# Optimization experiments

Hardware: AMD Instinct MI355X
Metric: run time of the kernel (lower is better)

## Reference

```python
import jax, jax.numpy as jnp
import numpy as np

NUM_V, NUM_R, ARITY = 100000, 1000, 3
D, I, H = 128, 64, 128
B, N = 4096, 64


def setup_inputs() -> dict:
    key = jax.random.key(0)
    ks = jax.random.split(key, 11)
    return {
        "r": jax.random.randint(ks[0], (B, N), 0, NUM_R),
        "e": jax.random.randint(ks[1], (ARITY, B, N), 0, NUM_V),
        "V": jax.random.normal(ks[2], (NUM_V, D + I), dtype=jnp.float32),
        "R": jax.random.normal(ks[3], (NUM_R, D), dtype=jnp.float32),
        "P": jax.random.normal(ks[4], (ARITY, D), dtype=jnp.float32),
        "WV": jax.random.normal(ks[5], (D + I, H), dtype=jnp.float32) * (1.0 / np.sqrt(D + I)),
        "bV": jax.random.normal(ks[6], (H,), dtype=jnp.float32) * 0.01,
        "WR": jax.random.normal(ks[7], (D, H), dtype=jnp.float32) * (1.0 / np.sqrt(D)),
        "bR": jax.random.normal(ks[8], (H,), dtype=jnp.float32) * 0.01,
        "WP": jax.random.normal(ks[9], (D, H), dtype=jnp.float32) * (1.0 / np.sqrt(D)),
        "bP": jax.random.normal(ks[10], (H,), dtype=jnp.float32) * 0.01,
    }


def reference(r, e, V, R, P, WV, bV, WR, bR, WP, bP):
    # x = Rl(R[r]) : gather relation embeddings then project -> [B, N, H]
    x = jnp.einsum("bnd,dh->bnh", R[r], WR) + bR
    # Pl(P[i]) for all arity positions at once -> [A, H]
    pe = P @ WP + bP
    # Vl(V[e[i]]) for all positions: gather then project -> [A, B, N, H]
    ve = jnp.einsum("abnd,dh->abnh", V[e], WV) + bV
    # loop body x = x * Pl(P[i]) * Vl(V[e[i]]) == product over arity axis
    x = x * jnp.prod(pe[:, None, None, :] * ve, axis=0)
    # dropout is identity (p=0 / eval); reduce over neighbor axis
    return jnp.sum(x, axis=1)  # [B, H]
```

## Files before the change

### kernel.cpp

```cpp
#include <hip/hip_runtime.h>

#define NUM_V 100000
#define NUM_R 1000
#define ARITY 3
#define DD 128
#define DI 192
#define HH 128
#define BB 4096
#define NN 64

typedef __attribute__((ext_vector_type(4))) float f32x4;
typedef __attribute__((ext_vector_type(8))) _Float16 half8;
typedef __attribute__((ext_vector_type(2))) _Float16 half2v;

__global__ __launch_bounds__(832, 6) void gemm_fused(
    const float* __restrict__ A, const float* __restrict__ WV, const float* __restrict__ bV,
    const float* __restrict__ R, const float* __restrict__ WR, const float* __restrict__ bR,
    const float* __restrict__ P, const float* __restrict__ WP, const float* __restrict__ bP,
    _Float16* __restrict__ VWh, _Float16* __restrict__ RWh, float* __restrict__ peProd,
    int M) {
    __shared__ unsigned short bsm[24576];

    const int tid = threadIdx.x;
    const int l = tid & 63;
    const int wv = tid >> 6;
    const int bid = blockIdx.x;

    const int tile = wv * 512 + bid;
    const int rowbase = tile * 16;
    const bool active = rowbase < M;

    float bcol[8];
#pragma unroll
    for (int ct = 0; ct < 8; ++ct) bcol[ct] = bV[ct * 16 + (l & 15)];

    const float* aptr;
    {
        int rr = rowbase + (l & 15);
        if (rr >= M) rr = M - 1;
        aptr = A + (size_t)rr * DI + (l >> 4) * 8;
    }

    f32x4 acc[8];
#pragma unroll
    for (int ct = 0; ct < 8; ++ct) acc[ct] = (f32x4){0.f, 0.f, 0.f, 0.f};

    float4 va[3][2];
#define LOAD_A(buf, ks)                                      \
    do {                                                     \
        va[buf][0] = *(const float4*)(aptr + (ks) * 32);     \
        va[buf][1] = *(const float4*)(aptr + (ks) * 32 + 4); \
    } while (0)

    if (active) {
        LOAD_A(0, 0);
        LOAD_A(1, 1);
    }

    if (tid < 768) {
#pragma unroll
        for (int i = 0; i < 4; ++i) {
            const int g = i * 768 + tid;
            const int ks = g >> 9;
            const int ct = (g >> 6) & 7;
            const int ln = g & 63;
            const int col = ct * 16 + (ln & 15);
            const int kbase = ks * 32 + ((ln >> 4) << 3);
            half8 hv;
#pragma unroll
            for (int j = 0; j < 8; ++j)
                hv[j] = (_Float16)WV[(size_t)(kbase + j) * HH + col];
            *(half8*)&bsm[(size_t)g * 8] = hv;
        }
    }

    __syncthreads();

    if (active) {
#pragma unroll
        for (int ks = 0; ks < 6; ++ks) {
            const int cur = ks % 3;
            if (ks < 4) LOAD_A((ks + 2) % 3, ks + 2);

            half8 ah;
            {
                half8 t;
                t[0] = (_Float16)va[cur][0].x;
                t[1] = (_Float16)va[cur][0].y;
                t[2] = (_Float16)va[cur][0].z;
                t[3] = (_Float16)va[cur][0].w;
                t[4] = (_Float16)va[cur][1].x;
                t[5] = (_Float16)va[cur][1].y;
                t[6] = (_Float16)va[cur][1].z;
                t[7] = (_Float16)va[cur][1].w;
                ah = t;
            }

#pragma unroll
            for (int ct = 0; ct < 8; ++ct) {
                const int fb = (ks * 8 + ct) * 512;
                half8 bh = *(const half8*)&bsm[fb + l * 8];
                acc[ct] = __builtin_amdgcn_mfma_f32_16x16x32_f16(ah, bh, acc[ct], 0, 0, 0);
            }
        }

        const int rb = rowbase + (l >> 4) * 4;
#pragma unroll
        for (int j = 0; j < 4; ++j) {
            const int row = rb + j;
            if (row < M) {
#pragma unroll
                for (int ct = 0; ct < 8; ++ct)
                    VWh[(size_t)row * HH + ct * 16 + (l & 15)] = (_Float16)(acc[ct][j] + bcol[ct]);
            }
        }
    }
#undef LOAD_A

    if (bid < 500) {
        if (tid < 256) {
            const int row = bid * 2 + (tid >> 7);
            const int col = tid & 127;
            float a2 = bR[col];
            const float* Rr = R + (size_t)row * DD;
            for (int d = 0; d < DD; ++d) a2 += Rr[d] * WR[(size_t)d * HH + col];
            RWh[(size_t)row * HH + col] = (_Float16)a2;
        }
    } else if (bid == 511) {
        if (tid < HH) {
            const int h = tid;
            float prod = 1.0f;
            for (int a = 0; a < ARITY; ++a) {
                float a2 = bP[h];
                for (int d = 0; d < DD; ++d) a2 += P[a * DD + d] * WP[d * HH + h];
                prod *= a2;
            }
            peProd[h] = prod;
        }
    }
}

__global__ __launch_bounds__(256) void gather_kernel(const int* __restrict__ r,
                                                     const int* __restrict__ e,
                                                     const _Float16* __restrict__ VWh,
                                                     const _Float16* __restrict__ RWh,
                                                     const float* __restrict__ peProd,
                                                     float* __restrict__ out) {
    __shared__ int rIdx[NN];
    __shared__ int eIdx[ARITY][NN];
    __shared__ float4 partial[3][16][2];

    const int b = blockIdx.x;
    const int tid = threadIdx.x;

    if (tid < NN) {
        rIdx[tid] = r[b * NN + tid];
    } else {
        int t = tid - NN;
        eIdx[t >> 6][t & 63] = e[(size_t)(t >> 6) * BB * NN + b * NN + (t & 63)];
    }
    __syncthreads();

    const int lane = tid & 63;
    const int wv = tid >> 6;
    const int q = lane >> 4;
    const int ho = lane & 15;

    float acc8[8];
#pragma unroll
    for (int k = 0; k < 8; ++k) acc8[k] = 0.f;

#pragma unroll
    for (int it = 0; it < 4; ++it) {
        int n = it * 16 + wv * 4 + q;
        half8 rw = *(const half8*)(RWh + (size_t)rIdx[n] * HH + ho * 8);
        half8 v0 = *(const half8*)(VWh + (size_t)eIdx[0][n] * HH + ho * 8);
        half8 v1 = *(const half8*)(VWh + (size_t)eIdx[1][n] * HH + ho * 8);
        half8 v2 = *(const half8*)(VWh + (size_t)eIdx[2][n] * HH + ho * 8);
        half8 p = rw * v0;
        p = p * v1;
        p = p * v2;
#pragma unroll
        for (int k = 0; k < 8; ++k) acc8[k] += (float)p[k];
    }

#pragma unroll
    for (int k = 0; k < 8; ++k) {
        acc8[k] += __shfl_xor(acc8[k], 16);
        acc8[k] += __shfl_xor(acc8[k], 32);
    }

    if (wv > 0 && lane < 16) {
        partial[wv - 1][ho][0] = make_float4(acc8[0], acc8[1], acc8[2], acc8[3]);
        partial[wv - 1][ho][1] = make_float4(acc8[4], acc8[5], acc8[6], acc8[7]);
    }
    __syncthreads();
    if (wv == 0 && lane < 16) {
        float4 s0 = make_float4(acc8[0], acc8[1], acc8[2], acc8[3]);
        float4 s1 = make_float4(acc8[4], acc8[5], acc8[6], acc8[7]);
#pragma unroll
        for (int g = 0; g < 3; ++g) {
            float4 t0 = partial[g][ho][0], t1 = partial[g][ho][1];
            s0.x += t0.x; s0.y += t0.y; s0.z += t0.z; s0.w += t0.w;
            s1.x += t1.x; s1.y += t1.y; s1.z += t1.z; s1.w += t1.w;
        }
        float4 p0 = ((const float4*)peProd)[ho * 2];
        float4 p1 = ((const float4*)peProd)[ho * 2 + 1];
        ((float4*)(out + (size_t)b * HH))[ho * 2] =
            make_float4(s0.x * p0.x, s0.y * p0.y, s0.z * p0.z, s0.w * p0.w);
        ((float4*)(out + (size_t)b * HH))[ho * 2 + 1] =
            make_float4(s1.x * p1.x, s1.y * p1.y, s1.z * p1.z, s1.w * p1.w);
    }
}

extern "C" void kernel_launch(void* const* d_in, const int* in_sizes, int n_in,
                              void* d_out, int out_size, void* d_ws, size_t ws_size,
                              hipStream_t stream) {
    const int* r = (const int*)d_in[0];
    const int* e = (const int*)d_in[1];
    const float* V = (const float*)d_in[2];
    const float* R = (const float*)d_in[3];
    const float* P = (const float*)d_in[4];
    const float* WV = (const float*)d_in[5];
    const float* bV = (const float*)d_in[6];
    const float* WR = (const float*)d_in[7];
    const float* bR = (const float*)d_in[8];
    const float* WP = (const float*)d_in[9];
    const float* bP = (const float*)d_in[10];
    float* out = (float*)d_out;

    _Float16* VWh = (_Float16*)d_ws;
    _Float16* RWh = VWh + (size_t)NUM_V * HH;
    float* peProd = (float*)(RWh + (size_t)NUM_R * HH);

    gemm_fused<<<512, 832, 0, stream>>>(V, WV, bV, R, WR, bR, P, WP, bP,
                                        VWh, RWh, peProd, NUM_V);
    gather_kernel<<<BB, 256, 0, stream>>>(r, e, VWh, RWh, peProd, out);
}
```

Before: 60.15 us.

## Reshape GEMM grid to 8-wave blocks and prefetch all A slices up front

The projection GEMM now launches about 782 blocks of 512 threads, one 16-row tile per wave with contiguous tile indexing, in place of 512 blocks of 832 threads. All six K-slices of the A row are loaded into registers before the weight-to-LDS conversion, replacing the rolling three-buffer prefetch, so global latency overlaps the weight staging. The aim is better CU occupancy balance and more memory-level parallelism. In exchange, each block redoes the weight conversion into LDS, so that overhead grows with the larger block count, and register pressure rises.

```diff
diff --git a/kernel.cpp b/kernel.cpp
--- a/kernel.cpp
+++ b/kernel.cpp
@@ -13,7 +13,7 @@
 typedef __attribute__((ext_vector_type(8))) _Float16 half8;
 typedef __attribute__((ext_vector_type(2))) _Float16 half2v;
 
-__global__ __launch_bounds__(832, 6) void gemm_fused(
+__global__ __launch_bounds__(512, 4) void gemm_fused(
     const float* __restrict__ A, const float* __restrict__ WV, const float* __restrict__ bV,
     const float* __restrict__ R, const float* __restrict__ WR, const float* __restrict__ bR,
     const float* __restrict__ P, const float* __restrict__ WP, const float* __restrict__ bP,
@@ -26,13 +26,9 @@
     const int wv = tid >> 6;
     const int bid = blockIdx.x;
 
-    const int tile = wv * 512 + bid;
+    const int tile = bid * 8 + wv;
     const int rowbase = tile * 16;
     const bool active = rowbase < M;
-
-    float bcol[8];
-#pragma unroll
-    for (int ct = 0; ct < 8; ++ct) bcol[ct] = bV[ct * 16 + (l & 15)];
 
     const float* aptr;
     {
@@ -41,61 +37,55 @@
         aptr = A + (size_t)rr * DI + (l >> 4) * 8;
     }
 
-    f32x4 acc[8];
-#pragma unroll
-    for (int ct = 0; ct < 8; ++ct) acc[ct] = (f32x4){0.f, 0.f, 0.f, 0.f};
-
-    float4 va[3][2];
-#define LOAD_A(buf, ks)                                      \
-    do {                                                     \
-        va[buf][0] = *(const float4*)(aptr + (ks) * 32);     \
-        va[buf][1] = *(const float4*)(aptr + (ks) * 32 + 4); \
-    } while (0)
+    f32x4 va[6][2];
+#pragma unroll
+    for (int ks = 0; ks < 6; ++ks) {
+        va[ks][0] = *(const f32x4*)(aptr + ks * 32);
+        va[ks][1] = *(const f32x4*)(aptr + ks * 32 + 4);
+    }
+    __builtin_amdgcn_sched_barrier(0);
+
+    float bcol[8];
+#pragma unroll
+    for (int ct = 0; ct < 8; ++ct) bcol[ct] = bV[ct * 16 + (l & 15)];
+
+#pragma unroll
+    for (int i = 0; i < 6; ++i) {
+        const int g = i * 512 + tid;
+        const int ks = g >> 9;
+        const int ct = (g >> 6) & 7;
+        const int ln = g & 63;
+        const int col = ct * 16 + (ln & 15);
+        const int kbase = ks * 32 + ((ln >> 4) << 3);
+        half8 hv;
+#pragma unroll
+        for (int j = 0; j < 8; ++j)
+            hv[j] = (_Float16)WV[(size_t)(kbase + j) * HH + col];
+        *(half8*)&bsm[(size_t)g * 8] = hv;
+    }
+
+    __syncthreads();
 
     if (active) {
-        LOAD_A(0, 0);
-        LOAD_A(1, 1);
-    }
-
-    if (tid < 768) {
-#pragma unroll
-        for (int i = 0; i < 4; ++i) {
-            const int g = i * 768 + tid;
-            const int ks = g >> 9;
-            const int ct = (g >> 6) & 7;
-            const int ln = g & 63;
-            const int col = ct * 16 + (ln & 15);
-            const int kbase = ks * 32 + ((ln >> 4) << 3);
-            half8 hv;
-#pragma unroll
-            for (int j = 0; j < 8; ++j)
-                hv[j] = (_Float16)WV[(size_t)(kbase + j) * HH + col];
-            *(half8*)&bsm[(size_t)g * 8] = hv;
-        }
-    }
-
-    __syncthreads();
-
-    if (active) {
+        f32x4 acc[8];
+#pragma unroll
+        for (int ct = 0; ct < 8; ++ct) acc[ct] = (f32x4){0.f, 0.f, 0.f, 0.f};
+
 #pragma unroll
         for (int ks = 0; ks < 6; ++ks) {
-            const int cur = ks % 3;
-            if (ks < 4) LOAD_A((ks + 2) % 3, ks + 2);
-
             half8 ah;
             {
                 half8 t;
-                t[0] = (_Float16)va[cur][0].x;
-                t[1] = (_Float16)va[cur][0].y;
-                t[2] = (_Float16)va[cur][0].z;
-                t[3] = (_Float16)va[cur][0].w;
-                t[4] = (_Float16)va[cur][1].x;
-                t[5] = (_Float16)va[cur][1].y;
-                t[6] = (_Float16)va[cur][1].z;
-                t[7] = (_Float16)va[cur][1].w;
+                t[0] = (_Float16)va[ks][0].x;
+                t[1] = (_Float16)va[ks][0].y;
+                t[2] = (_Float16)va[ks][0].z;
+                t[3] = (_Float16)va[ks][0].w;
+                t[4] = (_Float16)va[ks][1].x;
+                t[5] = (_Float16)va[ks][1].y;
+                t[6] = (_Float16)va[ks][1].z;
+                t[7] = (_Float16)va[ks][1].w;
                 ah = t;
             }
-
 #pragma unroll
             for (int ct = 0; ct < 8; ++ct) {
                 const int fb = (ks * 8 + ct) * 512;
@@ -115,7 +105,6 @@
             }
         }
     }
-#undef LOAD_A
 
     if (bid < 500) {
         if (tid < 256) {
@@ -126,7 +115,7 @@
             for (int d = 0; d < DD; ++d) a2 += Rr[d] * WR[(size_t)d * HH + col];
             RWh[(size_t)row * HH + col] = (_Float16)a2;
         }
-    } else if (bid == 511) {
+    } else if (bid == 501) {
         if (tid < HH) {
             const int h = tid;
             float prod = 1.0f;
@@ -233,7 +222,8 @@
     _Float16* RWh = VWh + (size_t)NUM_V * HH;
     float* peProd = (float*)(RWh + (size_t)NUM_R * HH);
 
-    gemm_fused<<<512, 832, 0, stream>>>(V, WV, bV, R, WR, bR, P, WP, bP,
-                                        VWh, RWh, peProd, NUM_V);
+    const int tiles = (NUM_V + 15) / 16;
+    gemm_fused<<<(tiles + 7) / 8, 512, 0, stream>>>(V, WV, bV, R, WR, bR, P, WP, bP,
+                                                    VWh, RWh, peProd, NUM_V);
     gather_kernel<<<BB, 256, 0, stream>>>(r, e, VWh, RWh, peProd, out);
 }
```

Measured after the change: 57.48 us, median of 2. 1.05x faster.
